# Kernel tuning notes

Measured on AMD Instinct MI355X. Metric: run time of the kernel, lower is better.

## Reference

```python
import jax, jax.numpy as jnp
import numpy as np

N = 65536      # total nodes (512 graphs x 128 agents)
E = 524288     # total edges (avg degree 8)
NPG = 128      # nodes per graph
OBS = 256      # dim_in_node + dim_in_u
HID = 512      # hidden_dim
MID = 256      # dim_mid
LSTM = 256     # dim_lstm_out
DOUT = 128     # dim_out
DLAST = 128    # dim_last
RFM = 256      # rfm_hidden_dim
LH = 256       # last_hidden
ACT = 8        # act_dims


def setup_inputs() -> dict:
    key = jax.random.key(0)
    ks = jax.random.split(key, 30)

    def rn(k, shape, fan_in):
        return jax.random.normal(k, shape, jnp.float32) * (1.0 / np.sqrt(fan_in))

    src = jax.random.randint(ks[3], (E,), 0, N, jnp.int32)
    # keep edges inside each 128-node graph (batched-graph semantics)
    dst = (src // NPG) * NPG + jax.random.randint(ks[4], (E,), 0, NPG, jnp.int32)

    inp = {
        "obs": jax.random.normal(ks[0], (N, OBS), jnp.float32),
        "h0": jax.random.normal(ks[1], (N, LSTM), jnp.float32) * 0.1,
        "c0": jax.random.normal(ks[2], (N, LSTM), jnp.float32) * 0.1,
        "src": src,
        "dst": dst,
        # mlp1a / mlp1b
        "w1a": rn(ks[5], (HID, OBS), OBS), "b1a": jnp.zeros((HID,), jnp.float32),
        "w1b": rn(ks[6], (MID, HID), HID), "b1b": jnp.zeros((MID,), jnp.float32),
        # lstm1 (gate order i,f,g,o as in torch)
        "w_ih": rn(ks[7], (4 * LSTM, MID), MID), "b_ih": jnp.zeros((4 * LSTM,), jnp.float32),
        "w_hh": rn(ks[8], (4 * LSTM, LSTM), LSTM), "b_hh": jnp.zeros((4 * LSTM,), jnp.float32),
        # mlp1
        "w1": rn(ks[9], (DOUT, LSTM), LSTM), "b1": jnp.zeros((DOUT,), jnp.float32),
        # RFMBlock edge MLP (input = src_nf ++ dst_nf = 2*DOUT; edge_feat/u are 0-dim)
        "we": rn(ks[10], (RFM, 2 * DOUT), 2 * DOUT), "be": jnp.zeros((RFM,), jnp.float32),
        "we2": rn(ks[11], (DLAST, RFM), RFM), "be2": jnp.zeros((DLAST,), jnp.float32),
        # RFMBlock node MLP (input = node_feat ++ h = DOUT + DLAST)
        "wn": rn(ks[12], (RFM, DOUT + DLAST), DOUT + DLAST), "bn": jnp.zeros((RFM,), jnp.float32),
        "wn2": rn(ks[13], (DLAST, RFM), RFM), "bn2": jnp.zeros((DLAST,), jnp.float32),
        # readout
        "wr": rn(ks[14], (LH, DLAST), DLAST), "br": jnp.zeros((LH,), jnp.float32),
        "wr2": rn(ks[15], (ACT, LH), LH), "br2": jnp.zeros((ACT,), jnp.float32),
    }
    return inp


def reference(obs, h0, c0, src, dst,
              w1a, b1a, w1b, b1b, w_ih, b_ih, w_hh, b_hh, w1, b1,
              we, be, we2, be2, wn, bn, wn2, bn2, wr, br, wr2, br2):
    # node encoder: mlp1b(relu(mlp1a(obs)))
    x = jnp.maximum(obs @ w1a.T + b1a, 0.0) @ w1b.T + b1b            # [N, MID]
    # single-step LSTM (batch = N nodes, seq_len = 1)
    gates = x @ w_ih.T + h0 @ w_hh.T + (b_ih + b_hh)                 # [N, 4*LSTM]
    i, f, g, o = jnp.split(gates, 4, axis=-1)
    c1 = jax.nn.sigmoid(f) * c0 + jax.nn.sigmoid(i) * jnp.tanh(g)
    h1 = jax.nn.sigmoid(o) * jnp.tanh(c1)
    nf = jnp.maximum(h1, 0.0) @ w1.T + b1                            # [N, DOUT]

    # RFMBlock edge update: fc_edge2(relu(fc_edge([src_nf, dst_nf])))
    einp = jnp.concatenate([nf[src], nf[dst]], axis=-1)              # [E, 2*DOUT]
    ef = jnp.maximum(einp @ we.T + be, 0.0) @ we2.T + be2            # [E, DLAST]

    # message = edge_feat, reduce = sum over incoming edges (by dst)
    agg = jax.ops.segment_sum(ef, dst, num_segments=N)               # [N, DLAST]

    # RFMBlock node update: fc_node2(relu(fc_node([node_feat, h])))
    ninp = jnp.concatenate([nf, agg], axis=-1)                       # [N, DOUT+DLAST]
    nf2 = jnp.maximum(ninp @ wn.T + bn, 0.0) @ wn2.T + bn2           # [N, DLAST]

    # readout: mlp1_readout2(relu(mlp1_readout(n_out)))
    logits = jnp.maximum(nf2 @ wr.T + br, 0.0) @ wr2.T + br2         # [N, ACT]
    return logits, h1, c1
```

## Files before the change

kernel.cpp:

```cpp
#include <hip/hip_runtime.h>
#include <cstdint>
#include <cstddef>


#define NN 65536
#define NE 524288

typedef __bf16 bf16x8 __attribute__((ext_vector_type(8)));
typedef float  f32x4  __attribute__((ext_vector_type(4)));

__device__ __forceinline__ float bf2f(unsigned short u){
  union { unsigned int i; float f; } v; v.i = ((unsigned int)u) << 16; return v.f;
}
__device__ __forceinline__ unsigned short f2b(float f){
  union { float f; unsigned int i; } v; v.f = f;
  unsigned int r = v.i + 0x7FFFu + ((v.i >> 16) & 1u);
  return (unsigned short)(r >> 16);
}
__device__ __forceinline__ float sigm(float x){ return 1.f/(1.f+__expf(-x)); }


struct ConvArgs {
  const float* s[14];
  unsigned short* d[14];
  int n4[14];
  int cnt;
};

__global__ __launch_bounds__(256) void convert_kernel(ConvArgs a){
  int stride = gridDim.x * blockDim.x;
  int gid = blockIdx.x * blockDim.x + threadIdx.x;
  for (int seg = 0; seg < a.cnt; ++seg){
    const float4* s = (const float4*)a.s[seg];
    ushort4* d = (ushort4*)a.d[seg];
    int n4 = a.n4[seg];
    for (int i = gid; i < n4; i += stride){
      float4 v = s[i];
      ushort4 o; o.x=f2b(v.x); o.y=f2b(v.y); o.z=f2b(v.z); o.w=f2b(v.w);
      d[i] = o;
    }
  }
}

template<int ACT>
__global__ __launch_bounds__(256) void gemm_kernel(
    const unsigned short* __restrict__ A, int lda,
    const unsigned short* __restrict__ B, int K,
    const float* __restrict__ bias,
    unsigned short* __restrict__ C, int ldc)
{
  __shared__ alignas(16) unsigned short As[2048];
  __shared__ alignas(16) unsigned short Bs[2048];
  int t = threadIdx.x, wave = t >> 6, lane = t & 63;
  int m0 = blockIdx.x * 64, n0 = blockIdx.y * 64;

  f32x4 acc[4] = {};
  int row = t >> 2, chunk = t & 3;
  int sidx = ((row >> 4) << 9) + (chunk << 7) + ((row & 15) << 3);
  const unsigned short* Ap = A + (size_t)(m0 + row) * lda + chunk * 8;
  const unsigned short* Bp = B + (size_t)(n0 + row) * K + chunk * 8;

  for (int kt = 0; kt < K; kt += 32){
    __syncthreads();
    *(uint4*)&As[sidx] = *(const uint4*)(Ap + kt);
    *(uint4*)&Bs[sidx] = *(const uint4*)(Bp + kt);
    __syncthreads();
    bf16x8 a = *(const bf16x8*)&As[(wave << 9) + ((lane >> 4) << 7) + ((lane & 15) << 3)];
#pragma unroll
    for (int j = 0; j < 4; ++j){
      bf16x8 b = *(const bf16x8*)&Bs[(j << 9) + ((lane >> 4) << 7) + ((lane & 15) << 3)];
      acc[j] = __builtin_amdgcn_mfma_f32_16x16x32_bf16(a, b, acc[j], 0, 0, 0);
    }
  }

  int coll = lane & 15, rq = lane >> 4;
#pragma unroll
  for (int j = 0; j < 4; ++j){
    int col = n0 + j * 16 + coll;
    float bv = bias[col];
#pragma unroll
    for (int r = 0; r < 4; ++r){
      int rrow = m0 + wave * 16 + rq * 4 + r;
      float v = acc[j][r] + bv;
      if (ACT) v = fmaxf(v, 0.f);
      C[(size_t)rrow * ldc + col] = f2b(v);
    }
  }
}

__global__ __launch_bounds__(256) void gates_lstm_kernel(
    const unsigned short* __restrict__ Xb,
    const unsigned short* __restrict__ H0b,
    const unsigned short* __restrict__ Wih,
    const unsigned short* __restrict__ Whh,
    const float* __restrict__ b_ih, const float* __restrict__ b_hh,
    const float* __restrict__ c0,
    float* __restrict__ h1o, float* __restrict__ c1o,
    unsigned short* __restrict__ rb)
{
  __shared__ alignas(16) unsigned short As[2048];
  __shared__ alignas(16) unsigned short Bs[4][2048];
  int t = threadIdx.x, wave = t >> 6, lane = t & 63;
  int m0 = blockIdx.x * 64, cb = blockIdx.y * 64;

  f32x4 acc[4][4] = {};
  int row = t >> 2, chunk = t & 3;
  int sidx = ((row >> 4) << 9) + (chunk << 7) + ((row & 15) << 3);

  for (int kt = 0; kt < 512; kt += 32){
    const unsigned short* Ap = (kt < 256)
        ? (Xb  + (size_t)(m0 + row) * 256 + kt)
        : (H0b + (size_t)(m0 + row) * 256 + (kt - 256));
    __syncthreads();
    *(uint4*)&As[sidx] = *(const uint4*)(Ap + chunk * 8);
#pragma unroll
    for (int g = 0; g < 4; ++g){
      const unsigned short* Wp = (kt < 256)
          ? (Wih + (size_t)(g * 256 + cb + row) * 256 + kt)
          : (Whh + (size_t)(g * 256 + cb + row) * 256 + (kt - 256));
      *(uint4*)&Bs[g][sidx] = *(const uint4*)(Wp + chunk * 8);
    }
    __syncthreads();
    bf16x8 a = *(const bf16x8*)&As[(wave << 9) + ((lane >> 4) << 7) + ((lane & 15) << 3)];
#pragma unroll
    for (int g = 0; g < 4; ++g){
#pragma unroll
      for (int j = 0; j < 4; ++j){
        bf16x8 b = *(const bf16x8*)&Bs[g][(j << 9) + ((lane >> 4) << 7) + ((lane & 15) << 3)];
        acc[g][j] = __builtin_amdgcn_mfma_f32_16x16x32_bf16(a, b, acc[g][j], 0, 0, 0);
      }
    }
  }

  int coll = lane & 15, rq = lane >> 4;
#pragma unroll
  for (int j = 0; j < 4; ++j){
    int col = cb + j * 16 + coll;
    float bi  = b_ih[col]       + b_hh[col];
    float bff = b_ih[256 + col] + b_hh[256 + col];
    float bg  = b_ih[512 + col] + b_hh[512 + col];
    float bo  = b_ih[768 + col] + b_hh[768 + col];
#pragma unroll
    for (int r = 0; r < 4; ++r){
      int node = m0 + wave * 16 + rq * 4 + r;
      size_t off = (size_t)node * 256 + col;
      float iv = sigm(acc[0][j][r] + bi);
      float fv = sigm(acc[1][j][r] + bff);
      float gv = tanhf(acc[2][j][r] + bg);
      float ov = sigm(acc[3][j][r] + bo);
      float cv = fv * c0[off] + iv * gv;
      float hv = ov * tanhf(cv);
      h1o[off] = hv;
      c1o[off] = cv;
      rb[off] = f2b(fmaxf(hv, 0.f));
    }
  }
}

__global__ __launch_bounds__(256) void edge_kernel(
    const unsigned short* __restrict__ ninp,
    const int* __restrict__ src, const int* __restrict__ dst,
    const unsigned short* __restrict__ Web,
    const float* __restrict__ be,
    const unsigned short* __restrict__ We2b,
    const float* __restrict__ be2,
    float* __restrict__ agg)
{
  __shared__ alignas(16) unsigned short EH[64 * 256];
  __shared__ alignas(16) unsigned short Bs[8192];
  __shared__ int ssrc[64], sdst[64];

  int t = threadIdx.x, wave = t >> 6, lane = t & 63;
  int e0 = blockIdx.x * 64;
  if (t < 64){ ssrc[t] = src[e0 + t]; sdst[t] = dst[e0 + t]; }
  __syncthreads();

  {
    int e = t >> 2, part = t & 3;
    int sn = ssrc[e], dn = sdst[e];
#pragma unroll
    for (int ch = 0; ch < 8; ++ch){
      int k = part * 64 + ch * 8;
      int node = (k < 128) ? sn : dn;
      int col = k & 127;
      uint4 v = *(const uint4*)&ninp[(size_t)node * 256 + col];
      int idx = ((k >> 5) << 11) + ((e >> 4) << 9) + (((k >> 3) & 3) << 7) + ((e & 15) << 3);
      *(uint4*)&EH[idx] = v;
    }
  }

  int brow = t >> 2, bchunk = t & 3;

  f32x4 acc[16] = {};
  for (int kt = 0; kt < 256; kt += 32){
    __syncthreads();
#pragma unroll
    for (int p = 0; p < 4; ++p){
      int r = p * 64 + brow;
      uint4 v = *(const uint4*)&Web[(size_t)r * 256 + kt + bchunk * 8];
      int idx = ((r >> 4) << 9) + (bchunk << 7) + ((r & 15) << 3);
      *(uint4*)&Bs[idx] = v;
    }
    __syncthreads();
    bf16x8 a = *(const bf16x8*)&EH[((kt >> 5) << 11) + (wave << 9) + ((lane >> 4) << 7) + ((lane & 15) << 3)];
#pragma unroll
    for (int j = 0; j < 16; ++j){
      bf16x8 b = *(const bf16x8*)&Bs[(j << 9) + ((lane >> 4) << 7) + ((lane & 15) << 3)];
      acc[j] = __builtin_amdgcn_mfma_f32_16x16x32_bf16(a, b, acc[j], 0, 0, 0);
    }
  }

  __syncthreads();
  {
    int coll = lane & 15, rq = lane >> 4;
#pragma unroll
    for (int j = 0; j < 16; ++j){
      int col = j * 16 + coll;
      float bv = be[col];
#pragma unroll
      for (int r = 0; r < 4; ++r){
        int row = wave * 16 + rq * 4 + r;
        float v = fmaxf(acc[j][r] + bv, 0.f);
        int idx = ((col >> 5) << 11) + ((row >> 4) << 9) + (((col >> 3) & 3) << 7) + ((row & 15) << 3) + (col & 7);
        EH[idx] = f2b(v);
      }
    }
  }

  f32x4 acc2[8] = {};
  for (int kt = 0; kt < 256; kt += 32){
    __syncthreads();
#pragma unroll
    for (int p = 0; p < 2; ++p){
      int r = p * 64 + brow;
      uint4 v = *(const uint4*)&We2b[(size_t)r * 256 + kt + bchunk * 8];
      int idx = ((r >> 4) << 9) + (bchunk << 7) + ((r & 15) << 3);
      *(uint4*)&Bs[idx] = v;
    }
    __syncthreads();
    bf16x8 a = *(const bf16x8*)&EH[((kt >> 5) << 11) + (wave << 9) + ((lane >> 4) << 7) + ((lane & 15) << 3)];
#pragma unroll
    for (int j = 0; j < 8; ++j){
      bf16x8 b = *(const bf16x8*)&Bs[(j << 9) + ((lane >> 4) << 7) + ((lane & 15) << 3)];
      acc2[j] = __builtin_amdgcn_mfma_f32_16x16x32_bf16(a, b, acc2[j], 0, 0, 0);
    }
  }

  {
    int coll = lane & 15, rq = lane >> 4;
#pragma unroll
    for (int j = 0; j < 8; ++j){
      int col = j * 16 + coll;
      float bv = be2[col];
#pragma unroll
      for (int r = 0; r < 4; ++r){
        int erow = wave * 16 + rq * 4 + r;
        int d = sdst[erow];
        atomicAdd(&agg[(size_t)d * 128 + col], acc2[j][r] + bv);
      }
    }
  }
}

__global__ __launch_bounds__(256) void aggconv_kernel(
    const float* __restrict__ agg, unsigned short* __restrict__ ninp)
{
  int i = blockIdx.x * blockDim.x + threadIdx.x;
  int n = i >> 5, c = (i & 31) * 4;
  float4 v = *(const float4*)&agg[(size_t)n * 128 + c];
  ushort4 o; o.x=f2b(v.x); o.y=f2b(v.y); o.z=f2b(v.z); o.w=f2b(v.w);
  *(ushort4*)&ninp[(size_t)n * 256 + 128 + c] = o;
}

__global__ __launch_bounds__(256) void logits_kernel(
    const unsigned short* __restrict__ rh,
    const unsigned short* __restrict__ wr2b,
    const float* __restrict__ br2,
    float* __restrict__ out)
{
  __shared__ alignas(16) unsigned short W[2048];
  int t = threadIdx.x;
  *(uint4*)&W[t * 8] = *(const uint4*)&wr2b[t * 8];
  __syncthreads();
  int node = blockIdx.x * 32 + (t >> 3);
  int o = t & 7;
  const unsigned short* r = rh + (size_t)node * 256;
  float s = br2[o];
#pragma unroll
  for (int k = 0; k < 256; k += 8){
    uint4 av = *(const uint4*)&r[k];
    const unsigned short* ap = (const unsigned short*)&av;
#pragma unroll
    for (int i = 0; i < 8; ++i) s += bf2f(ap[i]) * bf2f(W[o * 256 + k + i]);
  }
  out[(size_t)node * 8 + o] = s;
}

extern "C" void kernel_launch(void* const* d_in, const int* in_sizes, int n_in,
                              void* d_out, int out_size, void* d_ws, size_t ws_size,
                              hipStream_t stream)
{
  (void)in_sizes; (void)n_in; (void)out_size; (void)ws_size;
  const float* obs = (const float*)d_in[0];
  const float* h0  = (const float*)d_in[1];
  const float* c0  = (const float*)d_in[2];
  const int*   src = (const int*)d_in[3];
  const int*   dst = (const int*)d_in[4];
  const float* w1a = (const float*)d_in[5];
  const float* b1a = (const float*)d_in[6];
  const float* w1b = (const float*)d_in[7];
  const float* b1b = (const float*)d_in[8];
  const float* wih = (const float*)d_in[9];
  const float* bih = (const float*)d_in[10];
  const float* whh = (const float*)d_in[11];
  const float* bhh = (const float*)d_in[12];
  const float* w1  = (const float*)d_in[13];
  const float* b1  = (const float*)d_in[14];
  const float* we  = (const float*)d_in[15];
  const float* be  = (const float*)d_in[16];
  const float* we2 = (const float*)d_in[17];
  const float* be2 = (const float*)d_in[18];
  const float* wn  = (const float*)d_in[19];
  const float* bn  = (const float*)d_in[20];
  const float* wn2 = (const float*)d_in[21];
  const float* bn2 = (const float*)d_in[22];
  const float* wr  = (const float*)d_in[23];
  const float* br  = (const float*)d_in[24];
  const float* wr2 = (const float*)d_in[25];
  const float* br2 = (const float*)d_in[26];

  char* ws = (char*)d_ws;
  typedef unsigned short u16;
  u16* w1a_b = (u16*)(ws + 0);
  u16* w1b_b = (u16*)(ws + 262144);
  u16* wih_b = (u16*)(ws + 524288);
  u16* whh_b = (u16*)(ws + 1048576);
  u16* w1_b  = (u16*)(ws + 1572864);
  u16* we_b  = (u16*)(ws + 1638400);
  u16* we2_b = (u16*)(ws + 1769472);
  u16* wn_b  = (u16*)(ws + 1835008);
  u16* wn2_b = (u16*)(ws + 1966080);
  u16* wr_b  = (u16*)(ws + 2031616);
  u16* wr2_b = (u16*)(ws + 2097152);
  char* RA = ws + 2101248;
  char* RB = ws + 35655680;
  char* RY = ws + 69210112;
  char* RN = ws + 136318976;

  u16* obs_b = (u16*)RA;
  u16* x_b   = (u16*)RA;
  float* agg = (float*)RA;
  u16* h0_b  = (u16*)RB;
  u16* hidn  = (u16*)RB;
  u16* rh    = (u16*)RB;
  u16* y1    = (u16*)RY;
  u16* rb    = (u16*)RY;
  u16* ninp  = (u16*)(RY + 33554432);
  u16* nf2   = (u16*)RN;

  float* logits = (float*)d_out;
  float* h1o = logits + (size_t)NN * 8;
  float* c1o = h1o + (size_t)NN * 256;

  ConvArgs ca;
  const float* ss[13] = {obs, h0, w1a, w1b, wih, whh, w1, we, we2, wn, wn2, wr, wr2};
  u16* dd[13] = {obs_b, h0_b, w1a_b, w1b_b, wih_b, whh_b, w1_b, we_b, we2_b, wn_b, wn2_b, wr_b, wr2_b};
  int nn[13] = {NN*256, NN*256, 512*256, 256*512, 1024*256, 1024*256, 128*256,
                256*256, 128*256, 256*256, 128*256, 256*128, 8*256};
  for (int i = 0; i < 13; ++i){ ca.s[i]=ss[i]; ca.d[i]=dd[i]; ca.n4[i]=nn[i]/4; }
  ca.cnt = 13;
  convert_kernel<<<2048, 256, 0, stream>>>(ca);

  gemm_kernel<1><<<dim3(NN/64, 8), 256, 0, stream>>>(obs_b, 256, w1a_b, 256, b1a, y1, 512);
  gemm_kernel<0><<<dim3(NN/64, 4), 256, 0, stream>>>(y1, 512, w1b_b, 512, b1b, x_b, 256);
  gates_lstm_kernel<<<dim3(NN/64, 4), 256, 0, stream>>>(
      x_b, h0_b, wih_b, whh_b, bih, bhh, c0, h1o, c1o, rb);
  gemm_kernel<0><<<dim3(NN/64, 2), 256, 0, stream>>>(rb, 256, w1_b, 256, b1, ninp, 256);
  hipMemsetAsync(agg, 0, (size_t)NN * 128 * 4, stream);
  edge_kernel<<<NE/64, 256, 0, stream>>>(ninp, src, dst, we_b, be, we2_b, be2, agg);
  aggconv_kernel<<<NN*32/256, 256, 0, stream>>>(agg, ninp);
  gemm_kernel<1><<<dim3(NN/64, 4), 256, 0, stream>>>(ninp, 256, wn_b, 256, bn, hidn, 256);
  gemm_kernel<0><<<dim3(NN/64, 2), 256, 0, stream>>>(hidn, 256, wn2_b, 256, bn2, nf2, 128);
  gemm_kernel<1><<<dim3(NN/64, 4), 256, 0, stream>>>(nf2, 128, wr_b, 128, br, rh, 256);
  logits_kernel<<<NN/32, 256, 0, stream>>>(rh, wr2_b, br2, logits);
}
```

Before: 1.071 ms.

## Factor edge MLP into per-node projections and CSR gather-sum with linear second layer

```diff
diff --git a/kernel.cpp b/kernel.cpp
--- a/kernel.cpp
+++ b/kernel.cpp
@@ -18,7 +18,6 @@
   return (unsigned short)(r >> 16);
 }
 __device__ __forceinline__ float sigm(float x){ return 1.f/(1.f+__expf(-x)); }
-
 
 struct ConvArgs {
   const float* s[14];
@@ -42,11 +41,12 @@
   }
 }
 
-template<int ACT>
+template<int ACT, int RSCALE>
 __global__ __launch_bounds__(256) void gemm_kernel(
     const unsigned short* __restrict__ A, int lda,
-    const unsigned short* __restrict__ B, int K,
+    const unsigned short* __restrict__ B, int ldb, int K,
     const float* __restrict__ bias,
+    const int* __restrict__ rs,
     unsigned short* __restrict__ C, int ldc)
 {
   __shared__ alignas(16) unsigned short As[2048];
@@ -58,7 +58,7 @@
   int row = t >> 2, chunk = t & 3;
   int sidx = ((row >> 4) << 9) + (chunk << 7) + ((row & 15) << 3);
   const unsigned short* Ap = A + (size_t)(m0 + row) * lda + chunk * 8;
-  const unsigned short* Bp = B + (size_t)(n0 + row) * K + chunk * 8;
+  const unsigned short* Bp = B + (size_t)(n0 + row) * ldb + chunk * 8;
 
   for (int kt = 0; kt < K; kt += 32){
     __syncthreads();
@@ -81,7 +81,8 @@
 #pragma unroll
     for (int r = 0; r < 4; ++r){
       int rrow = m0 + wave * 16 + rq * 4 + r;
-      float v = acc[j][r] + bv;
+      float scale = RSCALE ? (float)rs[rrow] : 1.0f;
+      float v = acc[j][r] + bv * scale;
       if (ACT) v = fmaxf(v, 0.f);
       C[(size_t)rrow * ldc + col] = f2b(v);
     }
@@ -157,119 +158,89 @@
   }
 }
 
-__global__ __launch_bounds__(256) void edge_kernel(
-    const unsigned short* __restrict__ ninp,
+__global__ __launch_bounds__(256) void hist_kernel(
+    const int* __restrict__ dst, int* __restrict__ hist)
+{
+  int e = blockIdx.x * 256 + threadIdx.x;
+  atomicAdd(&hist[dst[e]], 1);
+}
+
+__global__ __launch_bounds__(256) void scan1_kernel(
+    const int* __restrict__ hist, int* __restrict__ offs, int* __restrict__ bsum)
+{
+  __shared__ int s[256];
+  int b = blockIdx.x, t = threadIdx.x;
+  int v = hist[b * 256 + t];
+  s[t] = v; __syncthreads();
+  for (int d = 1; d < 256; d <<= 1){
+    int x = (t >= d) ? s[t - d] : 0;
+    __syncthreads();
+    s[t] += x;
+    __syncthreads();
+  }
+  offs[b * 256 + t] = s[t] - v;
+  if (t == 255) bsum[b] = s[255];
+}
+
+__global__ __launch_bounds__(256) void scan2_kernel(int* __restrict__ bsum){
+  __shared__ int s[256];
+  int t = threadIdx.x;
+  int v = bsum[t];
+  s[t] = v; __syncthreads();
+  for (int d = 1; d < 256; d <<= 1){
+    int x = (t >= d) ? s[t - d] : 0;
+    __syncthreads();
+    s[t] += x;
+    __syncthreads();
+  }
+  bsum[t] = s[t] - v;
+}
+
+__global__ __launch_bounds__(256) void scan3_kernel(
+    int* __restrict__ offs, const int* __restrict__ bsum, int* __restrict__ cursor)
+{
+  int i = blockIdx.x * 256 + threadIdx.x;
+  int v = offs[i] + bsum[blockIdx.x];
+  offs[i] = v;
+  cursor[i] = v;
+}
+
+__global__ __launch_bounds__(256) void scatter_kernel(
     const int* __restrict__ src, const int* __restrict__ dst,
-    const unsigned short* __restrict__ Web,
-    const float* __restrict__ be,
-    const unsigned short* __restrict__ We2b,
-    const float* __restrict__ be2,
-    float* __restrict__ agg)
-{
-  __shared__ alignas(16) unsigned short EH[64 * 256];
-  __shared__ alignas(16) unsigned short Bs[8192];
-  __shared__ int ssrc[64], sdst[64];
-
-  int t = threadIdx.x, wave = t >> 6, lane = t & 63;
-  int e0 = blockIdx.x * 64;
-  if (t < 64){ ssrc[t] = src[e0 + t]; sdst[t] = dst[e0 + t]; }
-  __syncthreads();
-
-  {
-    int e = t >> 2, part = t & 3;
-    int sn = ssrc[e], dn = sdst[e];
-#pragma unroll
-    for (int ch = 0; ch < 8; ++ch){
-      int k = part * 64 + ch * 8;
-      int node = (k < 128) ? sn : dn;
-      int col = k & 127;
-      uint4 v = *(const uint4*)&ninp[(size_t)node * 256 + col];
-      int idx = ((k >> 5) << 11) + ((e >> 4) << 9) + (((k >> 3) & 3) << 7) + ((e & 15) << 3);
-      *(uint4*)&EH[idx] = v;
-    }
-  }
-
-  int brow = t >> 2, bchunk = t & 3;
-
-  f32x4 acc[16] = {};
-  for (int kt = 0; kt < 256; kt += 32){
-    __syncthreads();
-#pragma unroll
-    for (int p = 0; p < 4; ++p){
-      int r = p * 64 + brow;
-      uint4 v = *(const uint4*)&Web[(size_t)r * 256 + kt + bchunk * 8];
-      int idx = ((r >> 4) << 9) + (bchunk << 7) + ((r & 15) << 3);
-      *(uint4*)&Bs[idx] = v;
-    }
-    __syncthreads();
-    bf16x8 a = *(const bf16x8*)&EH[((kt >> 5) << 11) + (wave << 9) + ((lane >> 4) << 7) + ((lane & 15) << 3)];
-#pragma unroll
-    for (int j = 0; j < 16; ++j){
-      bf16x8 b = *(const bf16x8*)&Bs[(j << 9) + ((lane >> 4) << 7) + ((lane & 15) << 3)];
-      acc[j] = __builtin_amdgcn_mfma_f32_16x16x32_bf16(a, b, acc[j], 0, 0, 0);
-    }
-  }
-
-  __syncthreads();
-  {
-    int coll = lane & 15, rq = lane >> 4;
-#pragma unroll
-    for (int j = 0; j < 16; ++j){
-      int col = j * 16 + coll;
-      float bv = be[col];
-#pragma unroll
-      for (int r = 0; r < 4; ++r){
-        int row = wave * 16 + rq * 4 + r;
-        float v = fmaxf(acc[j][r] + bv, 0.f);
-        int idx = ((col >> 5) << 11) + ((row >> 4) << 9) + (((col >> 3) & 3) << 7) + ((row & 15) << 3) + (col & 7);
-        EH[idx] = f2b(v);
-      }
-    }
-  }
-
-  f32x4 acc2[8] = {};
-  for (int kt = 0; kt < 256; kt += 32){
-    __syncthreads();
-#pragma unroll
-    for (int p = 0; p < 2; ++p){
-      int r = p * 64 + brow;
-      uint4 v = *(const uint4*)&We2b[(size_t)r * 256 + kt + bchunk * 8];
-      int idx = ((r >> 4) << 9) + (bchunk << 7) + ((r & 15) << 3);
-      *(uint4*)&Bs[idx] = v;
-    }
-    __syncthreads();
-    bf16x8 a = *(const bf16x8*)&EH[((kt >> 5) << 11) + (wave << 9) + ((lane >> 4) << 7) + ((lane & 15) << 3)];
-#pragma unroll
-    for (int j = 0; j < 8; ++j){
-      bf16x8 b = *(const bf16x8*)&Bs[(j << 9) + ((lane >> 4) << 7) + ((lane & 15) << 3)];
-      acc2[j] = __builtin_amdgcn_mfma_f32_16x16x32_bf16(a, b, acc2[j], 0, 0, 0);
-    }
-  }
-
-  {
-    int coll = lane & 15, rq = lane >> 4;
-#pragma unroll
-    for (int j = 0; j < 8; ++j){
-      int col = j * 16 + coll;
-      float bv = be2[col];
-#pragma unroll
-      for (int r = 0; r < 4; ++r){
-        int erow = wave * 16 + rq * 4 + r;
-        int d = sdst[erow];
-        atomicAdd(&agg[(size_t)d * 128 + col], acc2[j][r] + bv);
-      }
-    }
-  }
-}
-
-__global__ __launch_bounds__(256) void aggconv_kernel(
-    const float* __restrict__ agg, unsigned short* __restrict__ ninp)
-{
-  int i = blockIdx.x * blockDim.x + threadIdx.x;
-  int n = i >> 5, c = (i & 31) * 4;
-  float4 v = *(const float4*)&agg[(size_t)n * 128 + c];
-  ushort4 o; o.x=f2b(v.x); o.y=f2b(v.y); o.z=f2b(v.z); o.w=f2b(v.w);
-  *(ushort4*)&ninp[(size_t)n * 256 + 128 + c] = o;
+    int* __restrict__ cursor, int* __restrict__ sorted_src)
+{
+  int e = blockIdx.x * 256 + threadIdx.x;
+  int d = dst[e];
+  int pos = atomicAdd(&cursor[d], 1);
+  sorted_src[pos] = src[e];
+}
+
+__global__ __launch_bounds__(256) void edge_agg_kernel(
+    const unsigned short* __restrict__ P,
+    const unsigned short* __restrict__ Q,
+    const int* __restrict__ sorted_src,
+    const int* __restrict__ offs,
+    const int* __restrict__ cnt,
+    unsigned short* __restrict__ Hsum)
+{
+  int t = threadIdx.x;
+  int n = (blockIdx.x << 2) + (t >> 6);
+  int lane = t & 63;
+  int d0 = lane * 4;
+  int off = offs[n], c = cnt[n];
+  ushort4 qv = *(const ushort4*)&Q[(size_t)n * 256 + d0];
+  float q0 = bf2f(qv.x), q1 = bf2f(qv.y), q2 = bf2f(qv.z), q3 = bf2f(qv.w);
+  float a0 = 0.f, a1 = 0.f, a2 = 0.f, a3 = 0.f;
+  for (int i = 0; i < c; ++i){
+    int s = sorted_src[off + i];
+    ushort4 pv = *(const ushort4*)&P[(size_t)s * 256 + d0];
+    a0 += fmaxf(bf2f(pv.x) + q0, 0.f);
+    a1 += fmaxf(bf2f(pv.y) + q1, 0.f);
+    a2 += fmaxf(bf2f(pv.z) + q2, 0.f);
+    a3 += fmaxf(bf2f(pv.w) + q3, 0.f);
+  }
+  ushort4 o; o.x = f2b(a0); o.y = f2b(a1); o.z = f2b(a2); o.w = f2b(a3);
+  *(ushort4*)&Hsum[(size_t)n * 256 + d0] = o;
 }
 
 __global__ __launch_bounds__(256) void logits_kernel(
@@ -342,25 +313,36 @@
   u16* wn2_b = (u16*)(ws + 1966080);
   u16* wr_b  = (u16*)(ws + 2031616);
   u16* wr2_b = (u16*)(ws + 2097152);
-  char* RA = ws + 2101248;
-  char* RB = ws + 35655680;
-  char* RY = ws + 69210112;
-  char* RN = ws + 136318976;
+  float* zbias = (float*)(ws + 2101248);
+  int* hist    = (int*)(ws + 2103296);
+  int* offs    = (int*)(ws + 2365440);
+  int* cursor  = (int*)(ws + 2627584);
+  int* bsum    = (int*)(ws + 2889728);
+  int* ssrc    = (int*)(ws + 2890752);
+
+  char* RA = ws + 5242880;
+  char* RB = ws + 38797312;
+  char* RY = ws + 72351744;
 
   u16* obs_b = (u16*)RA;
   u16* x_b   = (u16*)RA;
-  float* agg = (float*)RA;
+  u16* P     = (u16*)RA;
+  u16* nf2   = (u16*)RA;
   u16* h0_b  = (u16*)RB;
+  u16* Hsum  = (u16*)RB;
   u16* hidn  = (u16*)RB;
   u16* rh    = (u16*)RB;
   u16* y1    = (u16*)RY;
   u16* rb    = (u16*)RY;
+  u16* Q     = (u16*)RY;
   u16* ninp  = (u16*)(RY + 33554432);
-  u16* nf2   = (u16*)RN;
 
   float* logits = (float*)d_out;
   float* h1o = logits + (size_t)NN * 8;
   float* c1o = h1o + (size_t)NN * 256;
+
+  (void)hipMemsetAsync(zbias, 0, 2048, stream);
+  (void)hipMemsetAsync(hist, 0, 65536 * 4, stream);
 
   ConvArgs ca;
   const float* ss[13] = {obs, h0, w1a, w1b, wih, whh, w1, we, we2, wn, wn2, wr, wr2};
@@ -371,16 +353,23 @@
   ca.cnt = 13;
   convert_kernel<<<2048, 256, 0, stream>>>(ca);
 
-  gemm_kernel<1><<<dim3(NN/64, 8), 256, 0, stream>>>(obs_b, 256, w1a_b, 256, b1a, y1, 512);
-  gemm_kernel<0><<<dim3(NN/64, 4), 256, 0, stream>>>(y1, 512, w1b_b, 512, b1b, x_b, 256);
+  hist_kernel<<<NE/256, 256, 0, stream>>>(dst, hist);
+  scan1_kernel<<<256, 256, 0, stream>>>(hist, offs, bsum);
+  scan2_kernel<<<1, 256, 0, stream>>>(bsum);
+  scan3_kernel<<<256, 256, 0, stream>>>(offs, bsum, cursor);
+  scatter_kernel<<<NE/256, 256, 0, stream>>>(src, dst, cursor, ssrc);
+
+  gemm_kernel<1,0><<<dim3(NN/64, 8), 256, 0, stream>>>(obs_b, 256, w1a_b, 256, 256, b1a, nullptr, y1, 512);
+  gemm_kernel<0,0><<<dim3(NN/64, 4), 256, 0, stream>>>(y1, 512, w1b_b, 512, 512, b1b, nullptr, x_b, 256);
   gates_lstm_kernel<<<dim3(NN/64, 4), 256, 0, stream>>>(
       x_b, h0_b, wih_b, whh_b, bih, bhh, c0, h1o, c1o, rb);
-  gemm_kernel<0><<<dim3(NN/64, 2), 256, 0, stream>>>(rb, 256, w1_b, 256, b1, ninp, 256);
-  hipMemsetAsync(agg, 0, (size_t)NN * 128 * 4, stream);
-  edge_kernel<<<NE/64, 256, 0, stream>>>(ninp, src, dst, we_b, be, we2_b, be2, agg);
-  aggconv_kernel<<<NN*32/256, 256, 0, stream>>>(agg, ninp);
-  gemm_kernel<1><<<dim3(NN/64, 4), 256, 0, stream>>>(ninp, 256, wn_b, 256, bn, hidn, 256);
-  gemm_kernel<0><<<dim3(NN/64, 2), 256, 0, stream>>>(hidn, 256, wn2_b, 256, bn2, nf2, 128);
-  gemm_kernel<1><<<dim3(NN/64, 4), 256, 0, stream>>>(nf2, 128, wr_b, 128, br, rh, 256);
+  gemm_kernel<0,0><<<dim3(NN/64, 2), 256, 0, stream>>>(rb, 256, w1_b, 256, 256, b1, nullptr, ninp, 256);
+  gemm_kernel<0,0><<<dim3(NN/64, 4), 256, 0, stream>>>(ninp, 256, we_b, 256, 128, zbias, nullptr, P, 256);
+  gemm_kernel<0,0><<<dim3(NN/64, 4), 256, 0, stream>>>(ninp, 256, we_b + 128, 256, 128, be, nullptr, Q, 256);
+  edge_agg_kernel<<<NN/4, 256, 0, stream>>>(P, Q, ssrc, offs, hist, Hsum);
+  gemm_kernel<0,1><<<dim3(NN/64, 2), 256, 0, stream>>>(Hsum, 256, we2_b, 256, 256, be2, hist, ninp + 128, 256);
+  gemm_kernel<1,0><<<dim3(NN/64, 4), 256, 0, stream>>>(ninp, 256, wn_b, 256, 256, bn, nullptr, hidn, 256);
+  gemm_kernel<0,0><<<dim3(NN/64, 2), 256, 0, stream>>>(hidn, 256, wn2_b, 256, 256, bn2, nullptr, nf2, 128);
+  gemm_kernel<1,0><<<dim3(NN/64, 4), 256, 0, stream>>>(nf2, 128, wr_b, 128, 128, br, nullptr, rh, 256);
   logits_kernel<<<NN/32, 256, 0, stream>>>(rh, wr2_b, br2, logits);
 }
```

Result: faster. 876.8 us (-18.1%).
